# Performance work log

Hardware: AMD Instinct MI355X
Metric: run time of the kernel (lower is better)

## Reference

```python
import jax, jax.numpy as jnp
import numpy as np

B, S, D = 2, 2048, 1024
E, K, F = 8, 2, 4 * 1024  # num_experts, top_k, fc_rate*embed_dim
T = B * S


def setup_inputs() -> dict:
    key = jax.random.key(0)
    ks = jax.random.split(key, 8)
    w = lambda k, shape: jax.random.normal(k, shape, jnp.float32) * 0.02
    return {
        "hidden_states": jax.random.normal(ks[0], (B, S, D), jnp.float32),
        "noise": jax.random.normal(ks[1], (T, E), jnp.float32),  # randn_like in router
        "Wg": w(ks[2], (D, E)), "bg": jnp.zeros((E,), jnp.float32),
        "Wn": w(ks[3], (D, E)), "bn": jnp.zeros((E,), jnp.float32),
        "W1": w(ks[4], (E, D, F)), "b1": jnp.zeros((E, F), jnp.float32),
        "W2": w(ks[5], (E, F, D)), "b2": jnp.zeros((E, D), jnp.float32),
    }


def reference(hidden_states, noise, Wg, bg, Wn, bn, W1, b1, W2, b2):
    b, s, d = hidden_states.shape
    x = hidden_states.reshape(-1, d)  # [T, D]

    # --- NoisyTopkRouter ---
    gate_logits = x @ Wg + bg                        # [T, E]
    noise_logits = x @ Wn + bn                       # [T, E]
    noisy_logits = gate_logits + noise * jax.nn.softplus(noise_logits)
    rw = jax.nn.softmax(noisy_logits.astype(jnp.float32), axis=-1)
    top_w, top_i = jax.lax.top_k(rw, K)              # [T, K]
    top_w = top_w / top_w.sum(-1, keepdims=True)
    top_w = top_w.astype(x.dtype)

    # Dense per-token combine coefficients: coef[t,e] = sum_k top_w[t,k]*[top_i[t,k]==e]
    tok = jnp.arange(x.shape[0])[:, None]
    coef = jnp.zeros((x.shape[0], E), x.dtype).at[tok, top_i].add(top_w)  # [T, E]

    # --- Experts: Linear -> GELU(exact) -> Linear (dropout = identity, eval mode) ---
    h = jax.nn.gelu(jnp.einsum('td,edf->tef', x, W1) + b1, approximate=False)  # [T,E,F]
    y = jnp.einsum('tef,efd->ted', h, W2) + b2                                  # [T,E,D]
    out = jnp.einsum('ted,te->td', y, coef)                                     # [T,D]

    return out.reshape(b, s, d), noisy_logits, gate_logits
```

## Files before the change

kernel.cpp:

```cpp
#include <hip/hip_runtime.h>
#include <hip/hip_bf16.h>

#define T_TOK 4096
#define D_DIM 1024
#define E_NUM 8
#define F_DIM 4096
#define NPAIR 8192

#define BM 128
#define BN 128
#define BK 64

typedef float f32x4 __attribute__((ext_vector_type(4)));
typedef __bf16 bf16x8 __attribute__((ext_vector_type(8)));
typedef unsigned short u16x8 __attribute__((ext_vector_type(8)));

__device__ __forceinline__ unsigned short f2bf(float f) {
    unsigned int u = __float_as_uint(f);
    u += 0x7fffu + ((u >> 16) & 1u);
    return (unsigned short)(u >> 16);
}

typedef const __attribute__((address_space(1))) void GV;
typedef __attribute__((address_space(3))) void LV;

__device__ __forceinline__ void load_lds16(const void* g, void* l) {
    __builtin_amdgcn_global_load_lds((GV*)g, (LV*)l, 16, 0, 0);
}

__device__ __forceinline__ bf16x8 lds_frag(const unsigned short* S, int row, int cs) {
    int byte = row * (BK * 2) + ((cs * 2) ^ ((row & 7) << 4));
    return *(const bf16x8*)((const char*)S + byte);
}

__global__ __launch_bounds__(256) void router_kernel(
    const float* __restrict__ x, const float* __restrict__ noise,
    const float* __restrict__ Wg, const float* __restrict__ bg,
    const float* __restrict__ Wn, const float* __restrict__ bn,
    float* __restrict__ out_noisy, float* __restrict__ out_gate,
    int* __restrict__ tk_idx, float* __restrict__ tk_w)
{
    int lane = threadIdx.x & 63;
    int t = blockIdx.x * 4 + (threadIdx.x >> 6);
    const float* xr = x + (size_t)t * D_DIM;

    float ag[E_NUM] = {}, an[E_NUM] = {};
    for (int it = 0; it < D_DIM / 64; ++it) {
        int d = it * 64 + lane;
        float xv = xr[d];
        float4 g0 = *(const float4*)(Wg + (size_t)d * E_NUM);
        float4 g1 = *(const float4*)(Wg + (size_t)d * E_NUM + 4);
        float4 m0 = *(const float4*)(Wn + (size_t)d * E_NUM);
        float4 m1 = *(const float4*)(Wn + (size_t)d * E_NUM + 4);
        ag[0] += xv * g0.x; ag[1] += xv * g0.y; ag[2] += xv * g0.z; ag[3] += xv * g0.w;
        ag[4] += xv * g1.x; ag[5] += xv * g1.y; ag[6] += xv * g1.z; ag[7] += xv * g1.w;
        an[0] += xv * m0.x; an[1] += xv * m0.y; an[2] += xv * m0.z; an[3] += xv * m0.w;
        an[4] += xv * m1.x; an[5] += xv * m1.y; an[6] += xv * m1.z; an[7] += xv * m1.w;
    }
    #pragma unroll
    for (int off = 32; off > 0; off >>= 1) {
        #pragma unroll
        for (int e = 0; e < E_NUM; ++e) {
            ag[e] += __shfl_xor(ag[e], off);
            an[e] += __shfl_xor(an[e], off);
        }
    }
    if (lane == 0) {
        float nz[E_NUM];
        #pragma unroll
        for (int e = 0; e < E_NUM; ++e) {
            float g = ag[e] + bg[e];
            float nn = an[e] + bn[e];
            float sp = fmaxf(nn, 0.f) + log1pf(expf(-fabsf(nn)));
            float z = g + noise[(size_t)t * E_NUM + e] * sp;
            out_gate[(size_t)t * E_NUM + e] = g;
            out_noisy[(size_t)t * E_NUM + e] = z;
            nz[e] = z;
        }
        int e0 = 0;
        #pragma unroll
        for (int e = 1; e < E_NUM; ++e) if (nz[e] > nz[e0]) e0 = e;
        int e1 = (e0 == 0) ? 1 : 0;
        #pragma unroll
        for (int e = 0; e < E_NUM; ++e) if (e != e0 && nz[e] > nz[e1]) e1 = e;
        float b = expf(nz[e1] - nz[e0]);
        float w0 = 1.f / (1.f + b);
        float w1 = b / (1.f + b);
        tk_idx[t * 2] = e0;  tk_idx[t * 2 + 1] = e1;
        tk_w[t * 2] = w0;    tk_w[t * 2 + 1] = w1;
    }
}

__global__ __launch_bounds__(256) void scan_scatter_kernel(
    const int* __restrict__ tk_idx,
    int* __restrict__ perm, int* __restrict__ meta)
{
    __shared__ int cnt[256][E_NUM];
    __shared__ int soff[E_NUM];
    int tid = threadIdx.x;
    const int PPT = NPAIR / 256;
    int p0 = tid * PPT;

    int c[E_NUM] = {};
    for (int i = 0; i < PPT; ++i) c[tk_idx[p0 + i]]++;
    #pragma unroll
    for (int e = 0; e < E_NUM; ++e) cnt[tid][e] = c[e];
    __syncthreads();

    if (tid < E_NUM) {
        int s = 0;
        for (int j = 0; j < 256; ++j) { int v = cnt[j][tid]; cnt[j][tid] = s; s += v; }
        soff[tid] = s;
    }
    __syncthreads();

    if (tid == 0) {
        int off = 0, nt = 0;
        for (int e = 0; e < E_NUM; ++e) {
            int ce = soff[e];
            meta[1 + e] = off;
            meta[9 + e] = ce;
            for (int j = 0; j < ce; j += BM) {
                meta[32 + nt]  = e;
                meta[160 + nt] = off + j;
                meta[288 + nt] = off + ce;
                nt++;
            }
            off += ce;
        }
        meta[0] = nt;
    }
    __syncthreads();
    if (tid < E_NUM) soff[tid] = meta[1 + tid];
    __syncthreads();

    int pos[E_NUM];
    #pragma unroll
    for (int e = 0; e < E_NUM; ++e) pos[e] = soff[e] + cnt[tid][e];
    for (int i = 0; i < PPT; ++i) {
        int e = tk_idx[p0 + i];
        perm[pos[e]++] = p0 + i;
    }
}

__global__ __launch_bounds__(256) void convert_x_kernel(
    const float* __restrict__ x, unsigned short* __restrict__ xb)
{
    size_t i = ((size_t)blockIdx.x * 256 + threadIdx.x) * 8;
    float4 a = *(const float4*)(x + i);
    float4 b = *(const float4*)(x + i + 4);
    u16x8 o;
    o[0] = f2bf(a.x); o[1] = f2bf(a.y); o[2] = f2bf(a.z); o[3] = f2bf(a.w);
    o[4] = f2bf(b.x); o[5] = f2bf(b.y); o[6] = f2bf(b.z); o[7] = f2bf(b.w);
    *(u16x8*)(xb + i) = o;
}

__global__ __launch_bounds__(256) void transpose_kernel(
    const float* __restrict__ W, unsigned short* __restrict__ WT, int R, int C)
{
    __shared__ float tile[32][33];
    int e = blockIdx.z;
    int c0 = blockIdx.x * 32, r0 = blockIdx.y * 32;
    int tx = threadIdx.x & 31, ty = threadIdx.x >> 5;
    const float* src = W + (size_t)e * R * C;
    #pragma unroll
    for (int i = 0; i < 4; ++i)
        tile[ty + 8 * i][tx] = src[(size_t)(r0 + ty + 8 * i) * C + c0 + tx];
    __syncthreads();
    unsigned short* dst = WT + (size_t)e * C * R;
    #pragma unroll
    for (int i = 0; i < 4; ++i)
        dst[(size_t)(c0 + ty + 8 * i) * R + r0 + tx] = f2bf(tile[tx][ty + 8 * i]);
}

__global__ __launch_bounds__(256) void fc1_kernel(
    const unsigned short* __restrict__ xb,
    const unsigned short* __restrict__ W1T,
    const float* __restrict__ b1,
    const int* __restrict__ perm,
    const int* __restrict__ meta,
    unsigned short* __restrict__ h)
{
    const int nwg = 71 * (F_DIM / BN);
    const int cpx = nwg >> 3;
    int bid = blockIdx.x;
    int wg = (bid & 7) * cpx + (bid >> 3);
    int tile = wg >> 5;
    int n0 = (wg & 31) * BN;
    if (tile >= meta[0]) return;
    int e    = meta[32 + tile];
    int rs   = meta[160 + tile];
    int rend = meta[288 + tile];

    __shared__ __align__(16) unsigned short As[2][BM * BK];
    __shared__ __align__(16) unsigned short Bs[2][BN * BK];

    int tid = threadIdx.x, lane = tid & 63, wv = tid >> 6;
    int wm = (wv >> 1) * 64, wn = (wv & 1) * 64;
    int csw = ((tid & 7) ^ ((tid >> 3) & 7)) * 8;

    const unsigned short* asrc[4];
    #pragma unroll
    for (int i = 0; i < 4; ++i) {
        int q = tid + i * 256;
        int pos = rs + (q >> 3); if (pos >= NPAIR) pos = NPAIR - 1;
        int t = perm[pos] >> 1;
        asrc[i] = xb + (size_t)t * D_DIM + csw;
    }
    const unsigned short* bbase = W1T + ((size_t)e * F_DIM + n0 + wv * 32 + (lane >> 3)) * D_DIM + csw;

    f32x4 acc[4][4] = {};

#define STAGE1(k0, b) do { \
    _Pragma("unroll") \
    for (int i_ = 0; i_ < 4; ++i_) \
        load_lds16(asrc[i_] + (k0), &As[b][(wv * 64 + i_ * 256) * 8]); \
    _Pragma("unroll") \
    for (int j_ = 0; j_ < 4; ++j_) \
        load_lds16(bbase + (size_t)(j_ * 8) * D_DIM + (k0), &Bs[b][(wv * 32 + j_ * 8) * BK]); \
} while (0)

    STAGE1(0, 0);
    const int NT = D_DIM / BK;
    #pragma unroll 2
    for (int t = 0; t < NT; ++t) {
        int cur = t & 1;
        if (t + 1 < NT) {
            STAGE1((t + 1) * BK, cur ^ 1);
            asm volatile("s_waitcnt vmcnt(8)" ::: "memory");
        } else {
            asm volatile("s_waitcnt vmcnt(0)" ::: "memory");
        }
        __builtin_amdgcn_s_barrier();
        const unsigned short* A = As[cur];
        const unsigned short* B = Bs[cur];
        #pragma unroll
        for (int kk = 0; kk < BK; kk += 32) {
            bf16x8 af[4], bf[4];
            #pragma unroll
            for (int m = 0; m < 4; ++m)
                af[m] = lds_frag(A, wm + m * 16 + (lane & 15), kk + (lane >> 4) * 8);
            #pragma unroll
            for (int n = 0; n < 4; ++n)
                bf[n] = lds_frag(B, wn + n * 16 + (lane & 15), kk + (lane >> 4) * 8);
            #pragma unroll
            for (int m = 0; m < 4; ++m)
                #pragma unroll
                for (int n = 0; n < 4; ++n)
                    acc[m][n] = __builtin_amdgcn_mfma_f32_16x16x32_bf16(af[m], bf[n], acc[m][n], 0, 0, 0);
        }
        asm volatile("s_waitcnt lgkmcnt(0)" ::: "memory");
        __builtin_amdgcn_s_barrier();
    }
#undef STAGE1

    #pragma unroll
    for (int m = 0; m < 4; ++m) {
        #pragma unroll
        for (int j = 0; j < 4; ++j) {
            int r = wm + m * 16 + (lane >> 4) * 4 + j;
            int pos = rs + r;
            if (pos >= rend) continue;
            #pragma unroll
            for (int n = 0; n < 4; ++n) {
                int col = n0 + wn + n * 16 + (lane & 15);
                float v = acc[m][n][j] + b1[e * F_DIM + col];
                v = 0.5f * v * (1.f + erff(v * 0.70710678118654752f));
                h[(size_t)pos * F_DIM + col] = f2bf(v);
            }
        }
    }
}

__global__ __launch_bounds__(256) void fc2_kernel(
    const unsigned short* __restrict__ h,
    const unsigned short* __restrict__ W2T,
    const float* __restrict__ b2,
    const int* __restrict__ perm,
    const float* __restrict__ tk_w,
    const int* __restrict__ meta,
    float* __restrict__ out)
{
    const int nwg = 71 * (D_DIM / BN);
    const int cpx = nwg >> 3;
    int bid = blockIdx.x;
    int wg = (bid & 7) * cpx + (bid >> 3);
    int tile = wg >> 3;
    int n0 = (wg & 7) * BN;
    if (tile >= meta[0]) return;
    int e    = meta[32 + tile];
    int rs   = meta[160 + tile];
    int rend = meta[288 + tile];

    __shared__ __align__(16) unsigned short As[2][BM * BK];
    __shared__ __align__(16) unsigned short Bs[2][BN * BK];

    int tid = threadIdx.x, lane = tid & 63, wv = tid >> 6;
    int wm = (wv >> 1) * 64, wn = (wv & 1) * 64;
    int csw = ((tid & 7) ^ ((tid >> 3) & 7)) * 8;

    const unsigned short* asrc[4];
    #pragma unroll
    for (int i = 0; i < 4; ++i) {
        int q = tid + i * 256;
        int pos = rs + (q >> 3); if (pos >= NPAIR) pos = NPAIR - 1;
        asrc[i] = h + (size_t)pos * F_DIM + csw;
    }
    const unsigned short* bbase = W2T + ((size_t)e * D_DIM + n0 + wv * 32 + (lane >> 3)) * F_DIM + csw;

    f32x4 acc[4][4] = {};

#define STAGE2(k0, b) do { \
    _Pragma("unroll") \
    for (int i_ = 0; i_ < 4; ++i_) \
        load_lds16(asrc[i_] + (k0), &As[b][(wv * 64 + i_ * 256) * 8]); \
    _Pragma("unroll") \
    for (int j_ = 0; j_ < 4; ++j_) \
        load_lds16(bbase + (size_t)(j_ * 8) * F_DIM + (k0), &Bs[b][(wv * 32 + j_ * 8) * BK]); \
} while (0)

    STAGE2(0, 0);
    const int NT = F_DIM / BK;
    #pragma unroll 2
    for (int t = 0; t < NT; ++t) {
        int cur = t & 1;
        if (t + 1 < NT) {
            STAGE2((t + 1) * BK, cur ^ 1);
            asm volatile("s_waitcnt vmcnt(8)" ::: "memory");
        } else {
            asm volatile("s_waitcnt vmcnt(0)" ::: "memory");
        }
        __builtin_amdgcn_s_barrier();
        const unsigned short* A = As[cur];
        const unsigned short* B = Bs[cur];
        #pragma unroll
        for (int kk = 0; kk < BK; kk += 32) {
            bf16x8 af[4], bf[4];
            #pragma unroll
            for (int m = 0; m < 4; ++m)
                af[m] = lds_frag(A, wm + m * 16 + (lane & 15), kk + (lane >> 4) * 8);
            #pragma unroll
            for (int n = 0; n < 4; ++n)
                bf[n] = lds_frag(B, wn + n * 16 + (lane & 15), kk + (lane >> 4) * 8);
            #pragma unroll
            for (int m = 0; m < 4; ++m)
                #pragma unroll
                for (int n = 0; n < 4; ++n)
                    acc[m][n] = __builtin_amdgcn_mfma_f32_16x16x32_bf16(af[m], bf[n], acc[m][n], 0, 0, 0);
        }
        asm volatile("s_waitcnt lgkmcnt(0)" ::: "memory");
        __builtin_amdgcn_s_barrier();
    }
#undef STAGE2

    #pragma unroll
    for (int m = 0; m < 4; ++m) {
        #pragma unroll
        for (int j = 0; j < 4; ++j) {
            int r = wm + m * 16 + (lane >> 4) * 4 + j;
            int pos = rs + r;
            if (pos >= rend) continue;
            int pr = perm[pos];
            int t = pr >> 1;
            float w = tk_w[pr];
            #pragma unroll
            for (int n = 0; n < 4; ++n) {
                int col = n0 + wn + n * 16 + (lane & 15);
                float v = (acc[m][n][j] + b2[e * D_DIM + col]) * w;
                atomicAdd(&out[(size_t)t * D_DIM + col], v);
            }
        }
    }
}

extern "C" void kernel_launch(void* const* d_in, const int* in_sizes, int n_in,
                              void* d_out, int out_size, void* d_ws, size_t ws_size,
                              hipStream_t stream)
{
    const float* x     = (const float*)d_in[0];
    const float* noise = (const float*)d_in[1];
    const float* Wg    = (const float*)d_in[2];
    const float* bg    = (const float*)d_in[3];
    const float* Wn    = (const float*)d_in[4];
    const float* bn    = (const float*)d_in[5];
    const float* W1    = (const float*)d_in[6];
    const float* b1    = (const float*)d_in[7];
    const float* W2    = (const float*)d_in[8];
    const float* b2    = (const float*)d_in[9];

    float* out       = (float*)d_out;
    float* out_noisy = out + (size_t)T_TOK * D_DIM;
    float* out_gate  = out_noisy + (size_t)T_TOK * E_NUM;

    char* ws = (char*)d_ws;
    int*   tk_idx = (int*)ws;
    float* tk_w   = (float*)(ws + 32768);
    int*   perm   = (int*)(ws + 65536);
    int*   meta   = (int*)(ws + 98304);
    size_t off = 131072;
    unsigned short* xb   = (unsigned short*)(ws + off); off += (size_t)T_TOK * D_DIM * 2;
    unsigned short* W1T  = (unsigned short*)(ws + off); off += (size_t)E_NUM * F_DIM * D_DIM * 2;
    unsigned short* W2T  = (unsigned short*)(ws + off); off += (size_t)E_NUM * D_DIM * F_DIM * 2;
    unsigned short* hbuf = (unsigned short*)(ws + off); off += (size_t)NPAIR * F_DIM * 2;

    hipMemsetAsync(d_out, 0, (size_t)out_size * sizeof(float), stream);

    router_kernel<<<T_TOK / 4, 256, 0, stream>>>(x, noise, Wg, bg, Wn, bn,
                                                 out_noisy, out_gate, tk_idx, tk_w);
    scan_scatter_kernel<<<1, 256, 0, stream>>>(tk_idx, perm, meta);
    convert_x_kernel<<<(T_TOK * D_DIM) / (256 * 8), 256, 0, stream>>>(x, xb);
    transpose_kernel<<<dim3(F_DIM / 32, D_DIM / 32, E_NUM), 256, 0, stream>>>(W1, W1T, D_DIM, F_DIM);
    transpose_kernel<<<dim3(D_DIM / 32, F_DIM / 32, E_NUM), 256, 0, stream>>>(W2, W2T, F_DIM, D_DIM);

    fc1_kernel<<<71 * (F_DIM / BN), 256, 0, stream>>>(xb, W1T, b1, perm, meta, hbuf);
    fc2_kernel<<<71 * (D_DIM / BN), 256, 0, stream>>>(hbuf, W2T, b2, perm, tk_w, meta, out);
}
```

Before: 505.9 us.

## Single-buffer LDS in expert GEMMs, raise occupancy, split-K fc2

Both expert GEMM kernels drop double-buffered LDS staging for a single buffer with a full wait before each tile, and request 4 workgroups per CU via launch bounds, so latency is hidden by occupancy instead of software pipelining. fc2 is also split into two K halves with twice the workgroups, to improve CU utilisation on its small grid. The halves combine through the existing atomic adds, and the bias is added only by the first half. This trades away intra-block load/compute overlap and doubles atomic traffic on the output.

```diff
diff --git a/kernel.cpp b/kernel.cpp
--- a/kernel.cpp
+++ b/kernel.cpp
@@ -173,7 +173,7 @@
         dst[(size_t)(c0 + ty + 8 * i) * R + r0 + tx] = f2bf(tile[tx][ty + 8 * i]);
 }
 
-__global__ __launch_bounds__(256) void fc1_kernel(
+__global__ __launch_bounds__(256, 4) void fc1_kernel(
     const unsigned short* __restrict__ xb,
     const unsigned short* __restrict__ W1T,
     const float* __restrict__ b1,
@@ -192,8 +192,8 @@
     int rs   = meta[160 + tile];
     int rend = meta[288 + tile];
 
-    __shared__ __align__(16) unsigned short As[2][BM * BK];
-    __shared__ __align__(16) unsigned short Bs[2][BN * BK];
+    __shared__ __align__(16) unsigned short As[BM * BK];
+    __shared__ __align__(16) unsigned short Bs[BN * BK];
 
     int tid = threadIdx.x, lane = tid & 63, wv = tid >> 6;
     int wm = (wv >> 1) * 64, wn = (wv & 1) * 64;
@@ -211,38 +211,26 @@
 
     f32x4 acc[4][4] = {};
 
-#define STAGE1(k0, b) do { \
-    _Pragma("unroll") \
-    for (int i_ = 0; i_ < 4; ++i_) \
-        load_lds16(asrc[i_] + (k0), &As[b][(wv * 64 + i_ * 256) * 8]); \
-    _Pragma("unroll") \
-    for (int j_ = 0; j_ < 4; ++j_) \
-        load_lds16(bbase + (size_t)(j_ * 8) * D_DIM + (k0), &Bs[b][(wv * 32 + j_ * 8) * BK]); \
-} while (0)
-
-    STAGE1(0, 0);
     const int NT = D_DIM / BK;
-    #pragma unroll 2
     for (int t = 0; t < NT; ++t) {
-        int cur = t & 1;
-        if (t + 1 < NT) {
-            STAGE1((t + 1) * BK, cur ^ 1);
-            asm volatile("s_waitcnt vmcnt(8)" ::: "memory");
-        } else {
-            asm volatile("s_waitcnt vmcnt(0)" ::: "memory");
-        }
+        int k0 = t * BK;
+        #pragma unroll
+        for (int i = 0; i < 4; ++i)
+            load_lds16(asrc[i] + k0, &As[(wv * 64 + i * 256) * 8]);
+        #pragma unroll
+        for (int j = 0; j < 4; ++j)
+            load_lds16(bbase + (size_t)(j * 8) * D_DIM + k0, &Bs[(wv * 32 + j * 8) * BK]);
+        asm volatile("s_waitcnt vmcnt(0)" ::: "memory");
         __builtin_amdgcn_s_barrier();
-        const unsigned short* A = As[cur];
-        const unsigned short* B = Bs[cur];
         #pragma unroll
         for (int kk = 0; kk < BK; kk += 32) {
             bf16x8 af[4], bf[4];
             #pragma unroll
             for (int m = 0; m < 4; ++m)
-                af[m] = lds_frag(A, wm + m * 16 + (lane & 15), kk + (lane >> 4) * 8);
+                af[m] = lds_frag(As, wm + m * 16 + (lane & 15), kk + (lane >> 4) * 8);
             #pragma unroll
             for (int n = 0; n < 4; ++n)
-                bf[n] = lds_frag(B, wn + n * 16 + (lane & 15), kk + (lane >> 4) * 8);
+                bf[n] = lds_frag(Bs, wn + n * 16 + (lane & 15), kk + (lane >> 4) * 8);
             #pragma unroll
             for (int m = 0; m < 4; ++m)
                 #pragma unroll
@@ -252,7 +240,6 @@
         asm volatile("s_waitcnt lgkmcnt(0)" ::: "memory");
         __builtin_amdgcn_s_barrier();
     }
-#undef STAGE1
 
     #pragma unroll
     for (int m = 0; m < 4; ++m) {
@@ -272,7 +259,7 @@
     }
 }
 
-__global__ __launch_bounds__(256) void fc2_kernel(
+__global__ __launch_bounds__(256, 4) void fc2_kernel(
     const unsigned short* __restrict__ h,
     const unsigned short* __restrict__ W2T,
     const float* __restrict__ b2,
@@ -281,19 +268,22 @@
     const int* __restrict__ meta,
     float* __restrict__ out)
 {
-    const int nwg = 71 * (D_DIM / BN);
+    const int nwg = 71 * (D_DIM / BN) * 2;
     const int cpx = nwg >> 3;
     int bid = blockIdx.x;
     int wg = (bid & 7) * cpx + (bid >> 3);
-    int tile = wg >> 3;
-    int n0 = (wg & 7) * BN;
+    int tile = wg >> 4;
+    int rem  = wg & 15;
+    int n0 = (rem >> 1) * BN;
+    int ks = rem & 1;
     if (tile >= meta[0]) return;
     int e    = meta[32 + tile];
     int rs   = meta[160 + tile];
     int rend = meta[288 + tile];
-
-    __shared__ __align__(16) unsigned short As[2][BM * BK];
-    __shared__ __align__(16) unsigned short Bs[2][BN * BK];
+    int kbeg = ks * (F_DIM / 2);
+
+    __shared__ __align__(16) unsigned short As[BM * BK];
+    __shared__ __align__(16) unsigned short Bs[BN * BK];
 
     int tid = threadIdx.x, lane = tid & 63, wv = tid >> 6;
     int wm = (wv >> 1) * 64, wn = (wv & 1) * 64;
@@ -304,44 +294,33 @@
     for (int i = 0; i < 4; ++i) {
         int q = tid + i * 256;
         int pos = rs + (q >> 3); if (pos >= NPAIR) pos = NPAIR - 1;
-        asrc[i] = h + (size_t)pos * F_DIM + csw;
-    }
-    const unsigned short* bbase = W2T + ((size_t)e * D_DIM + n0 + wv * 32 + (lane >> 3)) * F_DIM + csw;
+        asrc[i] = h + (size_t)pos * F_DIM + kbeg + csw;
+    }
+    const unsigned short* bbase = W2T + ((size_t)e * D_DIM + n0 + wv * 32 + (lane >> 3)) * F_DIM
+                                + kbeg + csw;
 
     f32x4 acc[4][4] = {};
 
-#define STAGE2(k0, b) do { \
-    _Pragma("unroll") \
-    for (int i_ = 0; i_ < 4; ++i_) \
-        load_lds16(asrc[i_] + (k0), &As[b][(wv * 64 + i_ * 256) * 8]); \
-    _Pragma("unroll") \
-    for (int j_ = 0; j_ < 4; ++j_) \
-        load_lds16(bbase + (size_t)(j_ * 8) * F_DIM + (k0), &Bs[b][(wv * 32 + j_ * 8) * BK]); \
-} while (0)
-
-    STAGE2(0, 0);
-    const int NT = F_DIM / BK;
-    #pragma unroll 2
+    const int NT = (F_DIM / 2) / BK;
     for (int t = 0; t < NT; ++t) {
-        int cur = t & 1;
-        if (t + 1 < NT) {
-            STAGE2((t + 1) * BK, cur ^ 1);
-            asm volatile("s_waitcnt vmcnt(8)" ::: "memory");
-        } else {
-            asm volatile("s_waitcnt vmcnt(0)" ::: "memory");
-        }
+        int k0 = t * BK;
+        #pragma unroll
+        for (int i = 0; i < 4; ++i)
+            load_lds16(asrc[i] + k0, &As[(wv * 64 + i * 256) * 8]);
+        #pragma unroll
+        for (int j = 0; j < 4; ++j)
+            load_lds16(bbase + (size_t)(j * 8) * F_DIM + k0, &Bs[(wv * 32 + j * 8) * BK]);
+        asm volatile("s_waitcnt vmcnt(0)" ::: "memory");
         __builtin_amdgcn_s_barrier();
-        const unsigned short* A = As[cur];
-        const unsigned short* B = Bs[cur];
         #pragma unroll
         for (int kk = 0; kk < BK; kk += 32) {
             bf16x8 af[4], bf[4];
             #pragma unroll
             for (int m = 0; m < 4; ++m)
-                af[m] = lds_frag(A, wm + m * 16 + (lane & 15), kk + (lane >> 4) * 8);
+                af[m] = lds_frag(As, wm + m * 16 + (lane & 15), kk + (lane >> 4) * 8);
             #pragma unroll
             for (int n = 0; n < 4; ++n)
-                bf[n] = lds_frag(B, wn + n * 16 + (lane & 15), kk + (lane >> 4) * 8);
+                bf[n] = lds_frag(Bs, wn + n * 16 + (lane & 15), kk + (lane >> 4) * 8);
             #pragma unroll
             for (int m = 0; m < 4; ++m)
                 #pragma unroll
@@ -351,7 +330,6 @@
         asm volatile("s_waitcnt lgkmcnt(0)" ::: "memory");
         __builtin_amdgcn_s_barrier();
     }
-#undef STAGE2
 
     #pragma unroll
     for (int m = 0; m < 4; ++m) {
@@ -366,7 +344,8 @@
             #pragma unroll
             for (int n = 0; n < 4; ++n) {
                 int col = n0 + wn + n * 16 + (lane & 15);
-                float v = (acc[m][n][j] + b2[e * D_DIM + col]) * w;
+                float base = (ks == 0) ? b2[e * D_DIM + col] : 0.f;
+                float v = (acc[m][n][j] + base) * w;
                 atomicAdd(&out[(size_t)t * D_DIM + col], v);
             }
         }
@@ -413,5 +392,5 @@
     transpose_kernel<<<dim3(D_DIM / 32, F_DIM / 32, E_NUM), 256, 0, stream>>>(W2, W2T, F_DIM, D_DIM);
 
     fc1_kernel<<<71 * (F_DIM / BN), 256, 0, stream>>>(xb, W1T, b1, perm, meta, hbuf);
-    fc2_kernel<<<71 * (D_DIM / BN), 256, 0, stream>>>(hbuf, W2T, b2, perm, tk_w, meta, out);
-}
+    fc2_kernel<<<71 * (D_DIM / BN) * 2, 256, 0, stream>>>(hbuf, W2T, b2, perm, tk_w, meta, out);
+}
```

Result: faster. 478.3 us (-5.5%).
